# Optimization experiments

Measured on AMD Instinct MI355X. Metric: run time of the kernel, lower is better.

Reference implementation:

```python
import jax, jax.numpy as jnp
import numpy as np

B, D, C = 16384, 1024, 2048

def setup_inputs() -> dict:
    key = jax.random.key(0)
    k1, k2 = jax.random.split(key)
    x = jax.random.normal(k1, (B, D), dtype=jnp.float32)
    # kaiming_normal_ with nonlinearity='relu': std = sqrt(2 / fan_in)
    W = jax.random.normal(k2, (C, D), dtype=jnp.float32) * jnp.sqrt(2.0 / D)
    return {"x": x, "W": W, "task_id": 0}

def reference(x, W, task_id):
    # Original: -(x[:, :, None] - W.T[None, :, :])**2 .mean(1)  -> [B, C]
    # Algebraic rewrite: -(||x||^2/D - 2*x.W^T/D + ||w||^2/D)
    d = jnp.asarray(x.shape[1], x.dtype)
    x2 = jnp.sum(x * x, axis=1, keepdims=True) / d          # [B, 1]
    w2 = jnp.sum(W * W, axis=1) / d                          # [C]
    cross = jnp.einsum('bd,cd->bc', x, W) * (2.0 / d)        # [B, C]
    return cross - x2 - w2[None, :]
```

## Files before the change

kernel.cpp:

```cpp
#include <hip/hip_runtime.h>
#include <hip/hip_bf16.h>
#include <stdint.h>

#define B_ROWS 16384
#define D_DIM  1024
#define C_DIM  2048

#define BM 128
#define BN 128
#define BK 64

typedef short bf16x8 __attribute__((ext_vector_type(8)));
typedef float f32x4  __attribute__((ext_vector_type(4)));

__global__ __launch_bounds__(256) void cvt_norm(const float* __restrict__ src,
                                                ushort* __restrict__ dst,
                                                float* __restrict__ norm) {
    const int row = blockIdx.x;
    const int t   = threadIdx.x;
    const float4 v = ((const float4*)(src + (size_t)row * D_DIM))[t];
    float s = v.x * v.x + v.y * v.y + v.z * v.z + v.w * v.w;

    ushort4 u;
    __hip_bfloat16 h;
    h = __float2bfloat16(v.x); u.x = *(const ushort*)&h;
    h = __float2bfloat16(v.y); u.y = *(const ushort*)&h;
    h = __float2bfloat16(v.z); u.z = *(const ushort*)&h;
    h = __float2bfloat16(v.w); u.w = *(const ushort*)&h;
    ((ushort4*)(dst + (size_t)row * D_DIM))[t] = u;

    #pragma unroll
    for (int o = 32; o > 0; o >>= 1) s += __shfl_down(s, o, 64);
    __shared__ float red[4];
    if ((t & 63) == 0) red[t >> 6] = s;
    __syncthreads();
    if (t == 0)
        norm[row] = (red[0] + red[1] + red[2] + red[3]) * (1.0f / (float)D_DIM);
}

__global__ __launch_bounds__(256) void gemm_epilogue(
        const ushort* __restrict__ xb, const ushort* __restrict__ wb,
        const float* __restrict__ x2, const float* __restrict__ w2,
        float* __restrict__ out) {
    __shared__ ushort As[BM * BK];
    __shared__ ushort Bs[BN * BK];

    const int tid  = threadIdx.x;
    const int lane = tid & 63;
    const int bx   = blockIdx.x;
    const int nTiles = C_DIM / BN;
    const int mBase  = (bx / nTiles) * BM;
    const int nBase  = (bx % nTiles) * BN;

    const int waveM = ((tid >> 6) >> 1) * 64;
    const int waveN = ((tid >> 6) & 1) * 64;

    f32x4 acc[4][4];
    #pragma unroll
    for (int mi = 0; mi < 4; ++mi)
        #pragma unroll
        for (int ni = 0; ni < 4; ++ni)
            acc[mi][ni] = (f32x4){0.f, 0.f, 0.f, 0.f};

    const ushort* aG = xb + (size_t)mBase * D_DIM;
    const ushort* bG = wb + (size_t)nBase * D_DIM;

    const int rsel = lane & 15;
    const int quad = lane >> 4;

    for (int kt = 0; kt < D_DIM; kt += BK) {
        #pragma unroll
        for (int j = 0; j < 4; ++j) {
            const int c    = j * 256 + tid;
            const int row  = c >> 3;
            const int koff = (c & 7) * 8;
            const int ldsb = (j * 256 + (tid & 192)) * 8;
            __builtin_amdgcn_global_load_lds(
                (const __attribute__((address_space(1))) void*)(aG + (size_t)row * D_DIM + kt + koff),
                (__attribute__((address_space(3))) void*)(As + ldsb), 16, 0, 0);
            __builtin_amdgcn_global_load_lds(
                (const __attribute__((address_space(1))) void*)(bG + (size_t)row * D_DIM + kt + koff),
                (__attribute__((address_space(3))) void*)(Bs + ldsb), 16, 0, 0);
        }
        __syncthreads();

        #pragma unroll
        for (int ks = 0; ks < 2; ++ks) {
            const int k0 = ks * 32;
            bf16x8 a[4], b[4];
            #pragma unroll
            for (int mi = 0; mi < 4; ++mi)
                a[mi] = *(const bf16x8*)(As + (waveM + mi * 16 + rsel) * BK + k0 + quad * 8);
            #pragma unroll
            for (int ni = 0; ni < 4; ++ni)
                b[ni] = *(const bf16x8*)(Bs + (waveN + ni * 16 + rsel) * BK + k0 + quad * 8);
            #pragma unroll
            for (int mi = 0; mi < 4; ++mi)
                #pragma unroll
                for (int ni = 0; ni < 4; ++ni)
                    acc[mi][ni] = __builtin_amdgcn_mfma_f32_16x16x32_bf16(
                        a[mi], b[ni], acc[mi][ni], 0, 0, 0);
        }
        __syncthreads();
    }

    const float scale = 2.0f / (float)D_DIM;
    const int col0 = nBase + waveN + rsel;
    const int row0 = mBase + waveM + quad * 4;

    float x2r[4][4];
    #pragma unroll
    for (int mi = 0; mi < 4; ++mi)
        #pragma unroll
        for (int r = 0; r < 4; ++r)
            x2r[mi][r] = x2[row0 + mi * 16 + r];

    #pragma unroll
    for (int ni = 0; ni < 4; ++ni) {
        const int c   = col0 + ni * 16;
        const float wc = w2[c];
        #pragma unroll
        for (int mi = 0; mi < 4; ++mi) {
            #pragma unroll
            for (int r = 0; r < 4; ++r) {
                const int rr = row0 + mi * 16 + r;
                out[(size_t)rr * C_DIM + c] = acc[mi][ni][r] * scale - x2r[mi][r] - wc;
            }
        }
    }
}

extern "C" void kernel_launch(void* const* d_in, const int* in_sizes, int n_in,
                              void* d_out, int out_size, void* d_ws, size_t ws_size,
                              hipStream_t stream) {
    const float* x = (const float*)d_in[0];
    const float* W = (const float*)d_in[1];
    float* out = (float*)d_out;

    char* ws = (char*)d_ws;
    ushort* xb = (ushort*)ws;
    ushort* wb = (ushort*)(ws + (size_t)B_ROWS * D_DIM * sizeof(ushort));
    float*  x2 = (float*)(ws + (size_t)(B_ROWS + C_DIM) * D_DIM * sizeof(ushort));
    float*  w2 = x2 + B_ROWS;

    cvt_norm<<<B_ROWS, 256, 0, stream>>>(x, xb, x2);
    cvt_norm<<<C_DIM, 256, 0, stream>>>(W, wb, w2);

    gemm_epilogue<<<(B_ROWS / BM) * (C_DIM / BN), 256, 0, stream>>>(xb, wb, x2, w2, out);
}
```

Baseline: 280.9 us.

## Swizzle LDS tiles, remap blocks across XCDs, merge conversion launches

Applies an XOR swizzle to the k-chunk index when loading A/B tiles into LDS, and applies the same swizzle on the MFMA operand reads, to cut LDS bank conflicts from the 128-byte row stride. Remaps block IDs so each of the 8 XCDs gets a contiguous range of output tiles, which should improve L2 reuse of shared A/B rows. Also merges the two conversion/norm kernel launches into one. The swizzle moves which global chunks each lane fetches but keeps the loads contiguous per row.

```diff
diff --git a/kernel.cpp b/kernel.cpp
--- a/kernel.cpp
+++ b/kernel.cpp
@@ -13,11 +13,16 @@
 typedef short bf16x8 __attribute__((ext_vector_type(8)));
 typedef float f32x4  __attribute__((ext_vector_type(4)));
 
-__global__ __launch_bounds__(256) void cvt_norm(const float* __restrict__ src,
-                                                ushort* __restrict__ dst,
-                                                float* __restrict__ norm) {
-    const int row = blockIdx.x;
-    const int t   = threadIdx.x;
+__global__ __launch_bounds__(256) void cvt_norm_all(
+        const float* __restrict__ x, const float* __restrict__ W,
+        ushort* __restrict__ xb, ushort* __restrict__ wb,
+        float* __restrict__ x2, float* __restrict__ w2) {
+    const int blk = blockIdx.x;
+    const float* src; ushort* dst; float* norm; int row;
+    if (blk < B_ROWS) { src = x; dst = xb; norm = x2; row = blk; }
+    else              { src = W; dst = wb; norm = w2; row = blk - B_ROWS; }
+
+    const int t = threadIdx.x;
     const float4 v = ((const float4*)(src + (size_t)row * D_DIM))[t];
     float s = v.x * v.x + v.y * v.y + v.z * v.z + v.w * v.w;
 
@@ -47,10 +52,11 @@
 
     const int tid  = threadIdx.x;
     const int lane = tid & 63;
-    const int bx   = blockIdx.x;
-    const int nTiles = C_DIM / BN;
-    const int mBase  = (bx / nTiles) * BM;
-    const int nBase  = (bx % nTiles) * BN;
+    const int nT   = C_DIM / BN;
+    const int per  = (B_ROWS / BM) * nT / 8;
+    const int wid  = (blockIdx.x & 7) * per + (blockIdx.x >> 3);
+    const int mBase = (wid / nT) * BM;
+    const int nBase = (wid % nT) * BN;
 
     const int waveM = ((tid >> 6) >> 1) * 64;
     const int waveN = ((tid >> 6) & 1) * 64;
@@ -67,33 +73,34 @@
 
     const int rsel = lane & 15;
     const int quad = lane >> 4;
+    const int rk   = rsel & 7;
 
     for (int kt = 0; kt < D_DIM; kt += BK) {
         #pragma unroll
         for (int j = 0; j < 4; ++j) {
             const int c    = j * 256 + tid;
             const int row  = c >> 3;
-            const int koff = (c & 7) * 8;
+            const int ksrc = (c & 7) ^ (row & 7);
             const int ldsb = (j * 256 + (tid & 192)) * 8;
             __builtin_amdgcn_global_load_lds(
-                (const __attribute__((address_space(1))) void*)(aG + (size_t)row * D_DIM + kt + koff),
+                (const __attribute__((address_space(1))) void*)(aG + (size_t)row * D_DIM + kt + ksrc * 8),
                 (__attribute__((address_space(3))) void*)(As + ldsb), 16, 0, 0);
             __builtin_amdgcn_global_load_lds(
-                (const __attribute__((address_space(1))) void*)(bG + (size_t)row * D_DIM + kt + koff),
+                (const __attribute__((address_space(1))) void*)(bG + (size_t)row * D_DIM + kt + ksrc * 8),
                 (__attribute__((address_space(3))) void*)(Bs + ldsb), 16, 0, 0);
         }
         __syncthreads();
 
         #pragma unroll
         for (int ks = 0; ks < 2; ++ks) {
-            const int k0 = ks * 32;
+            const int kph = ((ks * 4 + quad) ^ rk) * 8;
             bf16x8 a[4], b[4];
             #pragma unroll
             for (int mi = 0; mi < 4; ++mi)
-                a[mi] = *(const bf16x8*)(As + (waveM + mi * 16 + rsel) * BK + k0 + quad * 8);
+                a[mi] = *(const bf16x8*)(As + (waveM + mi * 16 + rsel) * BK + kph);
             #pragma unroll
             for (int ni = 0; ni < 4; ++ni)
-                b[ni] = *(const bf16x8*)(Bs + (waveN + ni * 16 + rsel) * BK + k0 + quad * 8);
+                b[ni] = *(const bf16x8*)(Bs + (waveN + ni * 16 + rsel) * BK + kph);
             #pragma unroll
             for (int mi = 0; mi < 4; ++mi)
                 #pragma unroll
@@ -117,7 +124,7 @@
 
     #pragma unroll
     for (int ni = 0; ni < 4; ++ni) {
-        const int c   = col0 + ni * 16;
+        const int c = col0 + ni * 16;
         const float wc = w2[c];
         #pragma unroll
         for (int mi = 0; mi < 4; ++mi) {
@@ -143,8 +150,6 @@
     float*  x2 = (float*)(ws + (size_t)(B_ROWS + C_DIM) * D_DIM * sizeof(ushort));
     float*  w2 = x2 + B_ROWS;
 
-    cvt_norm<<<B_ROWS, 256, 0, stream>>>(x, xb, x2);
-    cvt_norm<<<C_DIM, 256, 0, stream>>>(W, wb, w2);
-
+    cvt_norm_all<<<B_ROWS + C_DIM, 256, 0, stream>>>(x, W, xb, wb, x2, w2);
     gemm_epilogue<<<(B_ROWS / BM) * (C_DIM / BN), 256, 0, stream>>>(xb, wb, x2, w2, out);
 }
```

Result: faster. 267.3 us (-4.8%).
